# Kernel optimization log

Hardware: AMD Instinct MI355X
Metric: run time of the kernel (lower is better)

Reference implementation:

```python
import jax, jax.numpy as jnp
import numpy as np
from jax import lax

B, S, D = 1, 2048, 1280
H = 16
HD = D // H  # 80
L = 2
I = 5120
SCALE = HD ** -0.5
EPS = 1e-6
GH, GW = 64, 32  # patch grid: GH*GW == S
THETA = 10000.0


def _make_rope(dtype=jnp.float32):
    # 2D vision RoPE: half the rotary dims encode row position, half column.
    half = HD // 2  # 40
    inv_freq = 1.0 / (THETA ** (jnp.arange(0, half, 2, dtype=jnp.float32) / half))  # [20]
    hpos = jnp.repeat(jnp.arange(GH, dtype=jnp.float32), GW)  # [S]
    wpos = jnp.tile(jnp.arange(GW, dtype=jnp.float32), GH)    # [S]
    freqs = jnp.concatenate([hpos[:, None] * inv_freq, wpos[:, None] * inv_freq], axis=-1)  # [S, 40]
    emb = jnp.concatenate([freqs, freqs], axis=-1)  # [S, 80]
    return jnp.cos(emb).astype(dtype), jnp.sin(emb).astype(dtype)


def setup_inputs() -> dict:
    key = jax.random.key(0)
    ks = jax.random.split(key, 8)
    cos, sin = _make_rope()
    std = 0.02
    return {
        "hidden_states": jax.random.normal(ks[0], (B, S, D), jnp.float32),
        "cos": cos,
        "sin": sin,
        "qkv_w": jax.random.normal(ks[1], (L, D, 3 * D), jnp.float32) * std,
        "qkv_b": jnp.zeros((L, 3 * D), jnp.float32),
        "proj_w": jax.random.normal(ks[2], (L, D, D), jnp.float32) * std,
        "proj_b": jnp.zeros((L, D), jnp.float32),
        "ln1_g": jnp.ones((L, D), jnp.float32),
        "ln1_b": jnp.zeros((L, D), jnp.float32),
        "ln2_g": jnp.ones((L, D), jnp.float32),
        "ln2_b": jnp.zeros((L, D), jnp.float32),
        "fc1_w": jax.random.normal(ks[3], (L, D, I), jnp.float32) * std,
        "fc1_b": jnp.zeros((L, I), jnp.float32),
        "fc2_w": jax.random.normal(ks[4], (L, I, D), jnp.float32) * std,
        "fc2_b": jnp.zeros((L, D), jnp.float32),
    }


def _layernorm(x, g, b):
    m = jnp.mean(x, axis=-1, keepdims=True)
    v = jnp.mean(jnp.square(x - m), axis=-1, keepdims=True)
    return (x - m) * lax.rsqrt(v + EPS) * g + b


def _rotate_half(x):
    h = x.shape[-1] // 2
    return jnp.concatenate([-x[..., h:], x[..., :h]], axis=-1)


def _block(x, cos, sin, p):
    (qkv_w, qkv_b, proj_w, proj_b, g1, b1, g2, b2, f1w, f1b, f2w, f2b) = p
    # --- attention ---
    h = _layernorm(x, g1, b1)
    qkv = h @ qkv_w + qkv_b                                    # [B,S,3D]
    qkv = qkv.reshape(B, S, 3, H, HD).transpose(2, 0, 3, 1, 4)  # [3,B,H,S,hd]
    q, k, v = qkv[0], qkv[1], qkv[2]
    q = q * cos + _rotate_half(q) * sin                        # cos/sin broadcast over B,H
    k = k * cos + _rotate_half(k) * sin
    scores = jnp.einsum("bhqd,bhkd->bhqk", q, k) * SCALE       # [B,H,S,S]
    w = jax.nn.softmax(scores.astype(jnp.float32), axis=-1).astype(x.dtype)
    o = jnp.einsum("bhqk,bhkd->bhqd", w, v)
    o = o.transpose(0, 2, 1, 3).reshape(B, S, D)
    x = x + (o @ proj_w + proj_b)
    # --- MLP ---
    h = _layernorm(x, g2, b2)
    x = x + jax.nn.gelu(h @ f1w + f1b, approximate=False) @ f2w + f2b
    return x


def reference(hidden_states, cos, sin, qkv_w, qkv_b, proj_w, proj_b,
              ln1_g, ln1_b, ln2_g, ln2_b, fc1_w, fc1_b, fc2_w, fc2_b):
    params = (qkv_w, qkv_b, proj_w, proj_b, ln1_g, ln1_b,
              ln2_g, ln2_b, fc1_w, fc1_b, fc2_w, fc2_b)

    def step(x, p):
        return _block(x, cos, sin, p), None

    out, _ = lax.scan(step, hidden_states, params)
    return out
```

## Files before the change

kernel.cpp:

```cpp
#include <hip/hip_runtime.h>
#include <hip/hip_bf16.h>

using bf16 = __hip_bfloat16;
using short8 = __attribute__((ext_vector_type(8))) short;
using f32x4  = __attribute__((ext_vector_type(4))) float;

#define GLDS16(g, l) __builtin_amdgcn_global_load_lds( \
    (const __attribute__((address_space(1))) void*)(g), \
    (__attribute__((address_space(3))) void*)(l), 16, 0, 0)

constexpr int S  = 2048;
constexpr int D  = 1280;
constexpr int H  = 16;
constexpr int HD = 80;
constexpr int IM = 5120;

__global__ __launch_bounds__(256) void transpose_w(const float* __restrict__ W,
                                                   bf16* __restrict__ Wt,
                                                   int K, int N) {
  __shared__ float t[32][33];
  int tx = threadIdx.x & 31, ty = threadIdx.x >> 5;
  int n0 = blockIdx.x * 32, k0 = blockIdx.y * 32;
#pragma unroll
  for (int i = 0; i < 4; i++)
    t[ty + i * 8][tx] = W[(size_t)(k0 + ty + i * 8) * N + n0 + tx];
  __syncthreads();
#pragma unroll
  for (int i = 0; i < 4; i++)
    Wt[(size_t)(n0 + ty + i * 8) * K + k0 + tx] = __float2bfloat16(t[tx][ty + i * 8]);
}

__global__ __launch_bounds__(256) void transpose_v(const bf16* __restrict__ v,
                                                   bf16* __restrict__ vt) {
  __shared__ bf16 t[16][17];
  int tx = threadIdx.x & 15, ty = threadIdx.x >> 4;
  int s0 = blockIdx.x * 16, d0 = blockIdx.y * 16, h = blockIdx.z;
  t[ty][tx] = v[(size_t)(h * S + s0 + ty) * HD + d0 + tx];
  __syncthreads();
  vt[(size_t)(h * HD + d0 + ty) * S + s0 + tx] = t[tx][ty];
}

__global__ __launch_bounds__(256) void layernorm_k(const float* __restrict__ x,
                                                   const float* __restrict__ g,
                                                   const float* __restrict__ b,
                                                   bf16* __restrict__ h) {
  int row = blockIdx.x, tid = threadIdx.x;
  const float* xr = x + (size_t)row * D;
  float v[5], s1 = 0.f, s2 = 0.f;
#pragma unroll
  for (int i = 0; i < 5; i++) {
    v[i] = xr[tid + i * 256];
    s1 += v[i]; s2 += v[i] * v[i];
  }
#pragma unroll
  for (int o = 32; o > 0; o >>= 1) {
    s1 += __shfl_down(s1, o);
    s2 += __shfl_down(s2, o);
  }
  __shared__ float r1[4], r2[4];
  if ((tid & 63) == 0) { r1[tid >> 6] = s1; r2[tid >> 6] = s2; }
  __syncthreads();
  s1 = r1[0] + r1[1] + r1[2] + r1[3];
  s2 = r2[0] + r2[1] + r2[2] + r2[3];
  float mean = s1 * (1.f / D);
  float rstd = rsqrtf(s2 * (1.f / D) - mean * mean + 1e-6f);
  bf16* hr = h + (size_t)row * D;
#pragma unroll
  for (int i = 0; i < 5; i++) {
    int c = tid + i * 256;
    hr[c] = __float2bfloat16((v[i] - mean) * rstd * g[c] + b[c]);
  }
}

__global__ __launch_bounds__(256) void rope_k(bf16* __restrict__ q, bf16* __restrict__ k,
                                              const float* __restrict__ cs,
                                              const float* __restrict__ sn) {
  int idx = blockIdx.x * 256 + threadIdx.x;
  int p  = idx % 40;
  int t  = idx / 40;
  int s  = t & (S - 1);
  int t2 = t >> 11;
  int hh = t2 & (H - 1);
  bf16* base = ((t2 >> 4) ? k : q) + (size_t)(hh * S + s) * HD;
  float c0 = cs[s * HD + p],      s0 = sn[s * HD + p];
  float c1 = cs[s * HD + p + 40], s1 = sn[s * HD + p + 40];
  float x0 = __bfloat162float(base[p]);
  float x1 = __bfloat162float(base[p + 40]);
  base[p]      = __float2bfloat16(x0 * c0 - x1 * s0);
  base[p + 40] = __float2bfloat16(x1 * c1 + x0 * s1);
}

template <int EPI, int N, int K, int SPLITK>
__global__ __launch_bounds__(256, 2) void gemm2(const bf16* __restrict__ A,
                                                const bf16* __restrict__ Bt,
                                                const float* __restrict__ bias,
                                                float* __restrict__ X,
                                                bf16* __restrict__ O,
                                                float* __restrict__ P) {
  __shared__ __align__(16) short As[2][128 * 32];
  __shared__ __align__(16) short Bs[2][128 * 32];
  int tid = threadIdx.x, lane = tid & 63, wid = tid >> 6;
  int l15 = lane & 15, l4 = lane >> 4;
  int wr = wid >> 1, wc = wid & 1;

  int gx = gridDim.x;
  int nwg = gx * (int)gridDim.y;
  int lin = blockIdx.y * gx + blockIdx.x;
  int q = nwg >> 3, r = nwg & 7;
  int xcd = lin & 7, idx = lin >> 3;
  int swz = (xcd < r ? xcd * (q + 1) : r * (q + 1) + (xcd - r) * q) + idx;
  int bx = swz % gx, by = swz / gx;

  int rowBase = by * 128, colBase = bx * 128;
  constexpr int KS = K / SPLITK;
  constexpr int NT = KS / 32;
  int k0 = blockIdx.z * KS;
  const bf16* Ab = A  + (size_t)rowBase * K + k0;
  const bf16* Bb = Bt + (size_t)colBase * K + k0;

  f32x4 acc[4][4] = {};

  auto stage = [&](int buf, int kt) {
#pragma unroll
    for (int i = 0; i < 2; i++) {
      int cb = wid * 128 + i * 64;
      int c  = cb + lane;
      int row = c >> 2;
      int ci  = (c & 3) ^ ((row >> 1) & 3);
      GLDS16(Ab + (size_t)row * K + kt * 32 + ci * 8, &As[buf][cb * 8]);
      GLDS16(Bb + (size_t)row * K + kt * 32 + ci * 8, &Bs[buf][cb * 8]);
    }
  };

  stage(0, 0);
  __syncthreads();

  int cur = 0;
  for (int kt = 0; kt < NT; kt++) {
    if (kt + 1 < NT) stage(cur ^ 1, kt + 1);
    short8 af[4], bfv[4];
    const short8* Av = (const short8*)As[cur];
    const short8* Bv = (const short8*)Bs[cur];
#pragma unroll
    for (int i = 0; i < 4; i++) {
      int ra = wr * 64 + i * 16 + l15;
      int rb = wc * 64 + i * 16 + l15;
      af[i]  = Av[ra * 4 + (l4 ^ ((ra >> 1) & 3))];
      bfv[i] = Bv[rb * 4 + (l4 ^ ((rb >> 1) & 3))];
    }
#pragma unroll
    for (int m = 0; m < 4; m++)
#pragma unroll
      for (int n = 0; n < 4; n++)
        acc[m][n] = __builtin_amdgcn_mfma_f32_16x16x32_bf16(af[m], bfv[n], acc[m][n], 0, 0, 0);
    __syncthreads();
    cur ^= 1;
  }

#pragma unroll
  for (int m = 0; m < 4; m++) {
#pragma unroll
    for (int n = 0; n < 4; n++) {
      int col = colBase + wc * 64 + n * 16 + l15;
      float bs = (EPI == 3) ? 0.f : bias[col];
      int row0 = rowBase + wr * 64 + m * 16 + l4 * 4;
#pragma unroll
      for (int j = 0; j < 4; j++) {
        float val = acc[m][n][j] + bs;
        int row = row0 + j;
        if (EPI == 0) {
          int which = col / D;
          int r2 = col - which * D;
          int hh = r2 / HD, d = r2 - hh * HD;
          O[(size_t)((which * H + hh) * S + row) * HD + d] = __float2bfloat16(val);
        } else if (EPI == 1) {
          X[(size_t)row * N + col] += val;
        } else if (EPI == 2) {
          float gl = 0.5f * val * (1.0f + erff(val * 0.70710678118654752f));
          O[(size_t)row * N + col] = __float2bfloat16(gl);
        } else {
          P[(size_t)blockIdx.z * (2048 * N) + (size_t)row * N + col] = val;
        }
      }
    }
  }
}

__global__ __launch_bounds__(256) void reduce_add(const float* __restrict__ P,
                                                  const float* __restrict__ bias,
                                                  float* __restrict__ X) {
  int i = blockIdx.x * 1024 + threadIdx.x * 4;
  int col = i % D;
  float4 p0 = *(const float4*)&P[i];
  float4 p1 = *(const float4*)&P[(size_t)2048 * D + i];
  float4 bv = *(const float4*)&bias[col];
  float4 xv = *(const float4*)&X[i];
  xv.x += p0.x + p1.x + bv.x;
  xv.y += p0.y + p1.y + bv.y;
  xv.z += p0.z + p1.z + bv.z;
  xv.w += p0.w + p1.w + bv.w;
  *(float4*)&X[i] = xv;
}

__global__ __launch_bounds__(256) void flash_k(const bf16* __restrict__ q,
                                               const bf16* __restrict__ k,
                                               const bf16* __restrict__ vt,
                                               bf16* __restrict__ o) {
  __shared__ __align__(16) bf16 Qs[128 * 80];
  __shared__ __align__(16) bf16 Ks[64 * 80];
  __shared__ __align__(16) bf16 Vts[80 * 64];
  __shared__ __align__(16) bf16 Ps[128 * 72];
  const float scale = 0.11180339887498949f;
  int tid = threadIdx.x, lane = tid & 63, wid = tid >> 6;
  int l15 = lane & 15, l4 = lane >> 4;
  int hh = blockIdx.y, qb = blockIdx.x * 128;

  const bf16* qg = q + (size_t)(hh * S + qb) * HD;
#pragma unroll
  for (int i = 0; i < 5; i++) {
    int cb = i * 256 + wid * 64;
    GLDS16(qg + (size_t)(cb + lane) * 8, Qs + cb * 8);
  }

  f32x4 oacc[2][5] = {};
  float mst[2][4], lst[2][4];
#pragma unroll
  for (int m = 0; m < 2; m++)
#pragma unroll
    for (int j = 0; j < 4; j++) { mst[m][j] = -3.0e38f; lst[m][j] = 0.f; }

  const short8 zero8 = {0, 0, 0, 0, 0, 0, 0, 0};
  __syncthreads();

  for (int kt = 0; kt < S / 64; kt++) {
    const bf16* kg = k + (size_t)(hh * S + kt * 64) * HD;
    const bf16* vg = vt + (size_t)hh * HD * S + kt * 64;
#pragma unroll
    for (int i = 0; i < 2; i++) {
      int cb = i * 256 + wid * 64;
      int c  = cb + lane;
      GLDS16(kg + c * 8, Ks + cb * 8);
      int hd = c >> 3, cc = (c & 7) ^ (hd & 7);
      GLDS16(vg + hd * S + cc * 8, Vts + cb * 8);
    }
    if (wid < 2) {
      int cb = 512 + wid * 64;
      int c  = cb + lane;
      GLDS16(kg + c * 8, Ks + cb * 8);
      int hd = c >> 3, cc = (c & 7) ^ (hd & 7);
      GLDS16(vg + hd * S + cc * 8, Vts + cb * 8);
    }
    __syncthreads();

    f32x4 sacc[2][4] = {};
#pragma unroll
    for (int kf = 0; kf < 3; kf++) {
      bool act = (kf < 2) || (l4 < 2);
      short8 aq[2], bk[4];
#pragma unroll
      for (int m = 0; m < 2; m++)
        aq[m] = act ? *(const short8*)&Qs[(wid * 32 + m * 16 + l15) * 80 + (kf * 4 + l4) * 8] : zero8;
#pragma unroll
      for (int n = 0; n < 4; n++)
        bk[n] = act ? *(const short8*)&Ks[(n * 16 + l15) * 80 + (kf * 4 + l4) * 8] : zero8;
#pragma unroll
      for (int m = 0; m < 2; m++)
#pragma unroll
        for (int n = 0; n < 4; n++)
          sacc[m][n] = __builtin_amdgcn_mfma_f32_16x16x32_bf16(aq[m], bk[n], sacc[m][n], 0, 0, 0);
    }

#pragma unroll
    for (int m = 0; m < 2; m++) {
#pragma unroll
      for (int j = 0; j < 4; j++) {
        float s0 = sacc[m][0][j] * scale, s1 = sacc[m][1][j] * scale;
        float s2 = sacc[m][2][j] * scale, s3 = sacc[m][3][j] * scale;
        float mx = fmaxf(fmaxf(s0, s1), fmaxf(s2, s3));
        mx = fmaxf(mx, __shfl_xor(mx, 1));
        mx = fmaxf(mx, __shfl_xor(mx, 2));
        mx = fmaxf(mx, __shfl_xor(mx, 4));
        mx = fmaxf(mx, __shfl_xor(mx, 8));
        float newm = fmaxf(mst[m][j], mx);
        float fac = __expf(mst[m][j] - newm);
        mst[m][j] = newm;
        float p0 = __expf(s0 - newm), p1 = __expf(s1 - newm);
        float p2 = __expf(s2 - newm), p3 = __expf(s3 - newm);
        int prow = wid * 32 + m * 16 + l4 * 4 + j;
        Ps[prow * 72 +      l15] = __float2bfloat16(p0);
        Ps[prow * 72 + 16 + l15] = __float2bfloat16(p1);
        Ps[prow * 72 + 32 + l15] = __float2bfloat16(p2);
        Ps[prow * 72 + 48 + l15] = __float2bfloat16(p3);
        float ps = p0 + p1 + p2 + p3;
        ps += __shfl_xor(ps, 1);
        ps += __shfl_xor(ps, 2);
        ps += __shfl_xor(ps, 4);
        ps += __shfl_xor(ps, 8);
        lst[m][j] = lst[m][j] * fac + ps;
#pragma unroll
        for (int n5 = 0; n5 < 5; n5++) oacc[m][n5][j] *= fac;
      }
    }

#pragma unroll
    for (int kf = 0; kf < 2; kf++) {
      short8 ap[2], bv[5];
#pragma unroll
      for (int m = 0; m < 2; m++)
        ap[m] = *(const short8*)&Ps[(wid * 32 + m * 16 + l15) * 72 + (kf * 4 + l4) * 8];
#pragma unroll
      for (int n5 = 0; n5 < 5; n5++) {
        int hd = n5 * 16 + l15;
        int cc = (kf * 4 + l4) ^ (hd & 7);
        bv[n5] = *(const short8*)&Vts[hd * 64 + cc * 8];
      }
#pragma unroll
      for (int m = 0; m < 2; m++)
#pragma unroll
        for (int n5 = 0; n5 < 5; n5++)
          oacc[m][n5] = __builtin_amdgcn_mfma_f32_16x16x32_bf16(ap[m], bv[n5], oacc[m][n5], 0, 0, 0);
    }
    __syncthreads();
  }

#pragma unroll
  for (int m = 0; m < 2; m++)
#pragma unroll
    for (int n5 = 0; n5 < 5; n5++)
#pragma unroll
      for (int j = 0; j < 4; j++) {
        int row = qb + wid * 32 + m * 16 + l4 * 4 + j;
        int col = hh * HD + n5 * 16 + l15;
        o[(size_t)row * D + col] = __float2bfloat16(oacc[m][n5][j] / lst[m][j]);
      }
}

extern "C" void kernel_launch(void* const* d_in, const int* in_sizes, int n_in,
                              void* d_out, int out_size, void* d_ws, size_t ws_size,
                              hipStream_t stream) {
  const float* hidden = (const float*)d_in[0];
  const float* cosp   = (const float*)d_in[1];
  const float* sinp   = (const float*)d_in[2];
  const float* qkv_w  = (const float*)d_in[3];
  const float* qkv_b  = (const float*)d_in[4];
  const float* proj_w = (const float*)d_in[5];
  const float* proj_b = (const float*)d_in[6];
  const float* ln1_g  = (const float*)d_in[7];
  const float* ln1_b  = (const float*)d_in[8];
  const float* ln2_g  = (const float*)d_in[9];
  const float* ln2_b  = (const float*)d_in[10];
  const float* fc1_w  = (const float*)d_in[11];
  const float* fc1_b  = (const float*)d_in[12];
  const float* fc2_w  = (const float*)d_in[13];
  const float* fc2_b  = (const float*)d_in[14];
  float* x = (float*)d_out;

  char* w = (char*)d_ws;
  auto alloc = [&](size_t bytes) { void* p = (void*)w; w += bytes; return p; };
  bf16* wqkvT  = (bf16*)alloc((size_t)3 * D * D * 2);
  bf16* wprojT = (bf16*)alloc((size_t)D * D * 2);
  bf16* wfc1T  = (bf16*)alloc((size_t)IM * D * 2);
  bf16* wfc2T  = (bf16*)alloc((size_t)D * IM * 2);
  bf16* hbuf   = (bf16*)alloc((size_t)S * D * 2);
  bf16* qkvb   = (bf16*)alloc((size_t)3 * H * S * HD * 2);
  bf16* vtbuf  = (bf16*)alloc((size_t)H * HD * S * 2);
  bf16* obuf   = (bf16*)alloc((size_t)S * D * 2);
  bf16* midb   = (bf16*)alloc((size_t)S * IM * 2);
  float* Pproj = (float*)midb;
  float* Pfc2  = (float*)qkvb;
  (void)ws_size; (void)in_sizes; (void)n_in; (void)out_size;

  hipMemcpyAsync(x, hidden, (size_t)S * D * sizeof(float), hipMemcpyDeviceToDevice, stream);

  for (int l = 0; l < 2; l++) {
    transpose_w<<<dim3(3 * D / 32, D / 32), 256, 0, stream>>>(qkv_w + (size_t)l * D * 3 * D, wqkvT, D, 3 * D);
    transpose_w<<<dim3(D / 32, D / 32), 256, 0, stream>>>(proj_w + (size_t)l * D * D, wprojT, D, D);
    transpose_w<<<dim3(IM / 32, D / 32), 256, 0, stream>>>(fc1_w + (size_t)l * D * IM, wfc1T, D, IM);
    transpose_w<<<dim3(D / 32, IM / 32), 256, 0, stream>>>(fc2_w + (size_t)l * IM * D, wfc2T, IM, D);

    layernorm_k<<<S, 256, 0, stream>>>(x, ln1_g + l * D, ln1_b + l * D, hbuf);
    gemm2<0, 3 * D, D, 1><<<dim3(3 * D / 128, S / 128, 1), 256, 0, stream>>>(
        hbuf, wqkvT, qkv_b + (size_t)l * 3 * D, nullptr, qkvb, nullptr);
    rope_k<<<(2 * H * S * (HD / 2)) / 256, 256, 0, stream>>>(
        qkvb, qkvb + (size_t)H * S * HD, cosp, sinp);
    transpose_v<<<dim3(S / 16, HD / 16, H), 256, 0, stream>>>(qkvb + (size_t)2 * H * S * HD, vtbuf);
    flash_k<<<dim3(S / 128, H), 256, 0, stream>>>(
        qkvb, qkvb + (size_t)H * S * HD, vtbuf, obuf);
    gemm2<3, D, D, 2><<<dim3(D / 128, S / 128, 2), 256, 0, stream>>>(
        obuf, wprojT, nullptr, nullptr, nullptr, Pproj);
    reduce_add<<<(S * D) / 1024, 256, 0, stream>>>(Pproj, proj_b + l * D, x);

    layernorm_k<<<S, 256, 0, stream>>>(x, ln2_g + l * D, ln2_b + l * D, hbuf);
    gemm2<2, IM, D, 1><<<dim3(IM / 128, S / 128, 1), 256, 0, stream>>>(
        hbuf, wfc1T, fc1_b + (size_t)l * IM, nullptr, midb, nullptr);
    gemm2<3, D, IM, 2><<<dim3(D / 128, S / 128, 2), 256, 0, stream>>>(
        midb, wfc2T, nullptr, nullptr, nullptr, Pfc2);
    reduce_add<<<(S * D) / 1024, 256, 0, stream>>>(Pfc2, fc2_b + l * D, x);
  }
}
```

Measured before the change: 802.3 us.

## Double-buffer K/V tiles in flash attention and shrink query tile to 64

```diff
diff --git a/kernel.cpp b/kernel.cpp
--- a/kernel.cpp
+++ b/kernel.cpp
@@ -206,133 +206,126 @@
                                                const bf16* __restrict__ k,
                                                const bf16* __restrict__ vt,
                                                bf16* __restrict__ o) {
-  __shared__ __align__(16) bf16 Qs[128 * 80];
-  __shared__ __align__(16) bf16 Ks[64 * 80];
-  __shared__ __align__(16) bf16 Vts[80 * 64];
-  __shared__ __align__(16) bf16 Ps[128 * 72];
+  __shared__ __align__(16) bf16 Qs[64 * 80];
+  __shared__ __align__(16) bf16 Ks[2][64 * 80];
+  __shared__ __align__(16) bf16 Vts[2][80 * 64];
+  __shared__ __align__(16) bf16 Ps[64 * 72];
   const float scale = 0.11180339887498949f;
   int tid = threadIdx.x, lane = tid & 63, wid = tid >> 6;
   int l15 = lane & 15, l4 = lane >> 4;
-  int hh = blockIdx.y, qb = blockIdx.x * 128;
+
+  int lin = blockIdx.y * 32 + blockIdx.x;
+  int swz = (lin & 7) * 64 + (lin >> 3);
+  int hh = swz >> 5, qb = (swz & 31) * 64;
 
   const bf16* qg = q + (size_t)(hh * S + qb) * HD;
 #pragma unroll
-  for (int i = 0; i < 5; i++) {
+  for (int i = 0; i < 2; i++) {
     int cb = i * 256 + wid * 64;
     GLDS16(qg + (size_t)(cb + lane) * 8, Qs + cb * 8);
   }
-
-  f32x4 oacc[2][5] = {};
-  float mst[2][4], lst[2][4];
-#pragma unroll
-  for (int m = 0; m < 2; m++)
-#pragma unroll
-    for (int j = 0; j < 4; j++) { mst[m][j] = -3.0e38f; lst[m][j] = 0.f; }
-
-  const short8 zero8 = {0, 0, 0, 0, 0, 0, 0, 0};
-  __syncthreads();
-
-  for (int kt = 0; kt < S / 64; kt++) {
+  if (wid < 2) {
+    int cb = 512 + wid * 64;
+    GLDS16(qg + (size_t)(cb + lane) * 8, Qs + cb * 8);
+  }
+
+  auto stage_kv = [&](int buf, int kt) {
     const bf16* kg = k + (size_t)(hh * S + kt * 64) * HD;
     const bf16* vg = vt + (size_t)hh * HD * S + kt * 64;
 #pragma unroll
     for (int i = 0; i < 2; i++) {
       int cb = i * 256 + wid * 64;
       int c  = cb + lane;
-      GLDS16(kg + c * 8, Ks + cb * 8);
-      int hd = c >> 3, cc = (c & 7) ^ (hd & 7);
-      GLDS16(vg + hd * S + cc * 8, Vts + cb * 8);
+      GLDS16(kg + (size_t)c * 8, &Ks[buf][cb * 8]);
+      int hd = c >> 3, ci = (c & 7) ^ (hd & 7);
+      GLDS16(vg + (size_t)hd * S + ci * 8, &Vts[buf][cb * 8]);
     }
     if (wid < 2) {
       int cb = 512 + wid * 64;
       int c  = cb + lane;
-      GLDS16(kg + c * 8, Ks + cb * 8);
-      int hd = c >> 3, cc = (c & 7) ^ (hd & 7);
-      GLDS16(vg + hd * S + cc * 8, Vts + cb * 8);
-    }
-    __syncthreads();
-
-    f32x4 sacc[2][4] = {};
+      GLDS16(kg + (size_t)c * 8, &Ks[buf][cb * 8]);
+      int hd = c >> 3, ci = (c & 7) ^ (hd & 7);
+      GLDS16(vg + (size_t)hd * S + ci * 8, &Vts[buf][cb * 8]);
+    }
+  };
+
+  f32x4 oacc[5] = {};
+  float mst[4], lst[4];
+#pragma unroll
+  for (int j = 0; j < 4; j++) { mst[j] = -3.0e38f; lst[j] = 0.f; }
+  const short8 zero8 = {0, 0, 0, 0, 0, 0, 0, 0};
+
+  stage_kv(0, 0);
+  __syncthreads();
+
+  int cur = 0;
+  for (int kt = 0; kt < S / 64; kt++) {
+    if (kt + 1 < S / 64) stage_kv(cur ^ 1, kt + 1);
+
+    f32x4 sacc[4] = {};
 #pragma unroll
     for (int kf = 0; kf < 3; kf++) {
       bool act = (kf < 2) || (l4 < 2);
-      short8 aq[2], bk[4];
-#pragma unroll
-      for (int m = 0; m < 2; m++)
-        aq[m] = act ? *(const short8*)&Qs[(wid * 32 + m * 16 + l15) * 80 + (kf * 4 + l4) * 8] : zero8;
-#pragma unroll
-      for (int n = 0; n < 4; n++)
-        bk[n] = act ? *(const short8*)&Ks[(n * 16 + l15) * 80 + (kf * 4 + l4) * 8] : zero8;
-#pragma unroll
-      for (int m = 0; m < 2; m++)
-#pragma unroll
-        for (int n = 0; n < 4; n++)
-          sacc[m][n] = __builtin_amdgcn_mfma_f32_16x16x32_bf16(aq[m], bk[n], sacc[m][n], 0, 0, 0);
-    }
-
-#pragma unroll
-    for (int m = 0; m < 2; m++) {
-#pragma unroll
-      for (int j = 0; j < 4; j++) {
-        float s0 = sacc[m][0][j] * scale, s1 = sacc[m][1][j] * scale;
-        float s2 = sacc[m][2][j] * scale, s3 = sacc[m][3][j] * scale;
-        float mx = fmaxf(fmaxf(s0, s1), fmaxf(s2, s3));
-        mx = fmaxf(mx, __shfl_xor(mx, 1));
-        mx = fmaxf(mx, __shfl_xor(mx, 2));
-        mx = fmaxf(mx, __shfl_xor(mx, 4));
-        mx = fmaxf(mx, __shfl_xor(mx, 8));
-        float newm = fmaxf(mst[m][j], mx);
-        float fac = __expf(mst[m][j] - newm);
-        mst[m][j] = newm;
-        float p0 = __expf(s0 - newm), p1 = __expf(s1 - newm);
-        float p2 = __expf(s2 - newm), p3 = __expf(s3 - newm);
-        int prow = wid * 32 + m * 16 + l4 * 4 + j;
-        Ps[prow * 72 +      l15] = __float2bfloat16(p0);
-        Ps[prow * 72 + 16 + l15] = __float2bfloat16(p1);
-        Ps[prow * 72 + 32 + l15] = __float2bfloat16(p2);
-        Ps[prow * 72 + 48 + l15] = __float2bfloat16(p3);
-        float ps = p0 + p1 + p2 + p3;
-        ps += __shfl_xor(ps, 1);
-        ps += __shfl_xor(ps, 2);
-        ps += __shfl_xor(ps, 4);
-        ps += __shfl_xor(ps, 8);
-        lst[m][j] = lst[m][j] * fac + ps;
-#pragma unroll
-        for (int n5 = 0; n5 < 5; n5++) oacc[m][n5][j] *= fac;
+      short8 aq = act ? *(const short8*)&Qs[(wid * 16 + l15) * 80 + (kf * 4 + l4) * 8] : zero8;
+#pragma unroll
+      for (int n = 0; n < 4; n++) {
+        short8 bk = act ? *(const short8*)&Ks[cur][(n * 16 + l15) * 80 + (kf * 4 + l4) * 8] : zero8;
+        sacc[n] = __builtin_amdgcn_mfma_f32_16x16x32_bf16(aq, bk, sacc[n], 0, 0, 0);
       }
     }
 
 #pragma unroll
+    for (int j = 0; j < 4; j++) {
+      float s0 = sacc[0][j] * scale, s1 = sacc[1][j] * scale;
+      float s2 = sacc[2][j] * scale, s3 = sacc[3][j] * scale;
+      float mx = fmaxf(fmaxf(s0, s1), fmaxf(s2, s3));
+      mx = fmaxf(mx, __shfl_xor(mx, 1));
+      mx = fmaxf(mx, __shfl_xor(mx, 2));
+      mx = fmaxf(mx, __shfl_xor(mx, 4));
+      mx = fmaxf(mx, __shfl_xor(mx, 8));
+      float newm = fmaxf(mst[j], mx);
+      float fac = __expf(mst[j] - newm);
+      mst[j] = newm;
+      float p0 = __expf(s0 - newm), p1 = __expf(s1 - newm);
+      float p2 = __expf(s2 - newm), p3 = __expf(s3 - newm);
+      int prow = wid * 16 + l4 * 4 + j;
+      Ps[prow * 72 +      l15] = __float2bfloat16(p0);
+      Ps[prow * 72 + 16 + l15] = __float2bfloat16(p1);
+      Ps[prow * 72 + 32 + l15] = __float2bfloat16(p2);
+      Ps[prow * 72 + 48 + l15] = __float2bfloat16(p3);
+      float ps = p0 + p1 + p2 + p3;
+      ps += __shfl_xor(ps, 1);
+      ps += __shfl_xor(ps, 2);
+      ps += __shfl_xor(ps, 4);
+      ps += __shfl_xor(ps, 8);
+      lst[j] = lst[j] * fac + ps;
+#pragma unroll
+      for (int n5 = 0; n5 < 5; n5++) oacc[n5][j] *= fac;
+    }
+
+#pragma unroll
     for (int kf = 0; kf < 2; kf++) {
-      short8 ap[2], bv[5];
-#pragma unroll
-      for (int m = 0; m < 2; m++)
-        ap[m] = *(const short8*)&Ps[(wid * 32 + m * 16 + l15) * 72 + (kf * 4 + l4) * 8];
+      short8 ap = *(const short8*)&Ps[(wid * 16 + l15) * 72 + (kf * 4 + l4) * 8];
 #pragma unroll
       for (int n5 = 0; n5 < 5; n5++) {
         int hd = n5 * 16 + l15;
         int cc = (kf * 4 + l4) ^ (hd & 7);
-        bv[n5] = *(const short8*)&Vts[hd * 64 + cc * 8];
+        short8 bv = *(const short8*)&Vts[cur][hd * 64 + cc * 8];
+        oacc[n5] = __builtin_amdgcn_mfma_f32_16x16x32_bf16(ap, bv, oacc[n5], 0, 0, 0);
       }
-#pragma unroll
-      for (int m = 0; m < 2; m++)
-#pragma unroll
-        for (int n5 = 0; n5 < 5; n5++)
-          oacc[m][n5] = __builtin_amdgcn_mfma_f32_16x16x32_bf16(ap[m], bv[n5], oacc[m][n5], 0, 0, 0);
     }
     __syncthreads();
-  }
-
-#pragma unroll
-  for (int m = 0; m < 2; m++)
-#pragma unroll
-    for (int n5 = 0; n5 < 5; n5++)
-#pragma unroll
-      for (int j = 0; j < 4; j++) {
-        int row = qb + wid * 32 + m * 16 + l4 * 4 + j;
-        int col = hh * HD + n5 * 16 + l15;
-        o[(size_t)row * D + col] = __float2bfloat16(oacc[m][n5][j] / lst[m][j]);
-      }
+    cur ^= 1;
+  }
+
+#pragma unroll
+  for (int n5 = 0; n5 < 5; n5++)
+#pragma unroll
+    for (int j = 0; j < 4; j++) {
+      int row = qb + wid * 16 + l4 * 4 + j;
+      int col = hh * HD + n5 * 16 + l15;
+      o[(size_t)row * D + col] = __float2bfloat16(oacc[n5][j] / lst[j]);
+    }
 }
 
 extern "C" void kernel_launch(void* const* d_in, const int* in_sizes, int n_in,
@@ -384,7 +377,7 @@
     rope_k<<<(2 * H * S * (HD / 2)) / 256, 256, 0, stream>>>(
         qkvb, qkvb + (size_t)H * S * HD, cosp, sinp);
     transpose_v<<<dim3(S / 16, HD / 16, H), 256, 0, stream>>>(qkvb + (size_t)2 * H * S * HD, vtbuf);
-    flash_k<<<dim3(S / 128, H), 256, 0, stream>>>(
+    flash_k<<<dim3(S / 64, H), 256, 0, stream>>>(
         qkvb, qkvb + (size_t)H * S * HD, vtbuf, obuf);
     gemm2<3, D, D, 2><<<dim3(D / 128, S / 128, 2), 256, 0, stream>>>(
         obuf, wprojT, nullptr, nullptr, nullptr, Pproj);
```

Result: faster. 758.9 us (-5.4%).
